# Kernel tuning notes

Hardware: AMD Instinct MI355X
Metric: run time of the kernel (lower is better)

The kernel has to match this reference:

```python
import jax, jax.numpy as jnp
import numpy as np
from jax import lax

PAD = 960          # tf.pad amount each side
LN_EPS = 1e-3      # keras LayerNormalization default epsilon


def _process(x, h, gamma, beta):
    """SmallConvNet: grouped 1D conv (per-channel learnable kernel) -> LayerNorm -> SiLU.
    x: (B, 2, 64), h: (2, 961) -> (B, 2, 1024). Dropout omitted (see notes)."""
    # grouped conv: each of the 2 'sequence' channels has its own length-961 kernel
    y = lax.conv_general_dilated(
        x, h[:, None, :],                 # kernel (O=2, I=1, W=961)
        window_strides=(1,), padding=[(PAD, PAD)],
        dimension_numbers=("NCH", "OIH", "NCH"),
        feature_group_count=2)            # (B, 2, 1024)
    mu = jnp.mean(y, axis=-1, keepdims=True)
    var = jnp.mean(jnp.square(y - mu), axis=-1, keepdims=True)
    ln = gamma * (y - mu) * lax.rsqrt(var + LN_EPS) + beta
    return jax.nn.silu(ln)


def reference(values, h, gamma, beta, symbols):
    # values: (B, 2, 64); symbols: (2, 64)
    vp = _process(values, h, gamma, beta)                              # (B, 2, 1024)
    sp = _process(jnp.zeros_like(values) + symbols, h, gamma, beta)    # (B, 2, 1024)
    # sign-based cosine-similarity attention: S[b,i,j] = mean_d sign(vp[b,j,d])*sign(vp[b,j,d]+sp[b,i,d])
    Xi = vp[:, None, :, :]   # (B, 1, N, D)
    Xj = sp[:, :, None, :]   # (B, N, 1, D)
    S = jnp.mean(jnp.sign(Xi) * jnp.sign(Xi + Xj), axis=-1)           # (B, N, N)
    scores = jax.nn.softmax(S, axis=-1)
    attn = jnp.einsum("bij,bjd->bid", scores, vp)                     # (B, N, D)
    return jax.nn.silu(attn * sp)


def setup_inputs() -> dict:
    key = jax.random.key(0)
    k1, k2, k3 = jax.random.split(key, 3)
    B, N, Din, D = 16384, 2, 64, 1024
    return {
        "values": jax.random.normal(k1, (B, N, Din), dtype=jnp.float32),
        "h": jax.random.normal(k2, (2, 961), dtype=jnp.float32),
        "gamma": jnp.ones((D,), dtype=jnp.float32),
        "beta": jnp.zeros((D,), dtype=jnp.float32),
        "symbols": jax.random.normal(k3, (N, Din), dtype=jnp.float32),
    }
```

## Files before the change

kernel.cpp:

```cpp
#include <hip/hip_runtime.h>

#define LN_EPS 1e-3f

typedef __attribute__((ext_vector_type(8))) short bf16x8;
typedef __attribute__((ext_vector_type(4))) float f32x4;

static __device__ __forceinline__ float sgnf(float x) {
    return (x > 0.f) ? 1.f : ((x < 0.f) ? -1.f : 0.f);
}
static __device__ __forceinline__ float siluf(float x) {
    return x * __builtin_amdgcn_rcpf(1.f + __expf(-x));
}

static __device__ __forceinline__ unsigned short f2bf(float f) {
    unsigned int u = __float_as_uint(f);
    return (unsigned short)((u + 0x7fffu + ((u >> 16) & 1u)) >> 16);
}
static __device__ __forceinline__ float bf2f(unsigned short s) {
    return __uint_as_float(((unsigned int)s) << 16);
}
static __device__ __forceinline__ void split3(float v, unsigned short& hi,
                                              unsigned short& mid, unsigned short& lo) {
    hi = f2bf(v);
    const float r1 = v - bf2f(hi);
    mid = f2bf(r1);
    const float r2 = r1 - bf2f(mid);
    lo = f2bf(r2);
}

#define SPOFF 196608

__global__ __launch_bounds__(256) void hd_prep_sp(
    const float* __restrict__ h, const float* __restrict__ symbols,
    const float* __restrict__ gamma, const float* __restrict__ beta,
    float* __restrict__ ws)
{
    __shared__ float h_pad[2][1088];
    __shared__ float x_s[2][64];
    __shared__ float red[4][2];
    const int t = threadIdx.x;

    for (int idx = t; idx < 2 * 1088; idx += 256) {
        const int c = idx / 1088, j = idx - c * 1088;
        float v = 0.f;
        if (j >= 63 && j <= 1023) v = h[c * 961 + (j - 63)];
        h_pad[c][j] = v;
    }
    if (t < 128) x_s[t >> 6][t & 63] = symbols[t];
    __syncthreads();

    const int c = t >> 7, tt = t & 127;
    const int lane = t & 63, wid = t >> 6;
    const int jbase = 1023 - tt;

    float acc[8];
    #pragma unroll
    for (int k = 0; k < 8; ++k) acc[k] = 0.f;

    #pragma unroll 8
    for (int i = 0; i < 64; ++i) {
        const float xv = x_s[c][i];
        #pragma unroll
        for (int k = 0; k < 8; ++k)
            acc[k] = fmaf(xv, h_pad[c][jbase + i - 128 * k], acc[k]);
    }

    float ps = 0.f, pq = 0.f;
    #pragma unroll
    for (int k = 0; k < 8; ++k) { ps += acc[k]; pq += acc[k] * acc[k]; }
    #pragma unroll
    for (int off = 32; off; off >>= 1) {
        ps += __shfl_xor(ps, off);
        pq += __shfl_xor(pq, off);
    }
    if (lane == 0) { red[wid][0] = ps; red[wid][1] = pq; }
    __syncthreads();

    const float sum = red[2 * c][0] + red[2 * c + 1][0];
    const float sq  = red[2 * c][1] + red[2 * c + 1][1];
    const float mu  = sum * (1.f / 1024.f);
    float var = sq * (1.f / 1024.f) - mu * mu;
    var = fmaxf(var, 0.f);
    const float rs = rsqrtf(var + LN_EPS);

    #pragma unroll
    for (int k = 0; k < 8; ++k) {
        const int d = tt + 128 * k;
        const float ln = (acc[k] - mu) * rs * gamma[d] + beta[d];
        ws[SPOFF + c * 1024 + d] = siluf(ln);
    }
}

__global__ __launch_bounds__(256) void hd_prep_bpack(
    const float* __restrict__ h, float* __restrict__ ws)
{
    unsigned short* Bp = (unsigned short*)ws;
    const int total = 2 * 2 * 64 * 64 * 8;
    for (int e = blockIdx.x * 256 + threadIdx.x; e < total; e += gridDim.x * 256) {
        const int j   = e & 7;
        const int l   = (e >> 3) & 63;
        const int ntg = (e >> 9) & 63;
        const int ks  = (e >> 15) & 1;
        const int c   = (e >> 16) & 1;
        const int H = 1023 - (16 * ntg + (l & 15)) + 32 * ks + 8 * (l >> 4) + j;
        float v = 0.f;
        if (H >= 63 && H <= 1023) v = h[c * 961 + (H - 63)];
        unsigned short hi, mid, lo;
        split3(v, hi, mid, lo);
        const int T = (c * 2 + ks) * 64 + ntg;
        Bp[((T * 192 +   0 + l)) * 8 + j] = hi;
        Bp[((T * 192 +  64 + l)) * 8 + j] = mid;
        Bp[((T * 192 + 128 + l)) * 8 + j] = lo;
    }
}

__global__ __launch_bounds__(1024, 4) void hd_main_mfma(
    const float* __restrict__ values,
    const float* __restrict__ gamma, const float* __restrict__ beta,
    const float* __restrict__ ws, float* __restrict__ out)
{
    __shared__ __align__(16) unsigned short a_lds[2][2][3][16][40];
    __shared__ float stats[16][4][2][4][2];
    __shared__ float statsF[64];
    __shared__ int   sredF [64];
    __shared__ float otile[16][4][72];

    const int t = threadIdx.x;
    const int w = t >> 6, l = t & 63;
    const int g = l >> 4, q = l & 15;
    const int b0 = blockIdx.x * 16;

    if (t < 64) sredF[t] = 0;

    {
        const float2 xv2 = *reinterpret_cast<const float2*>(
            values + (size_t)b0 * 128 + 2 * t);
        #pragma unroll
        for (int u = 0; u < 2; ++u) {
            const int v  = 2 * t + u;
            const int q_ = v >> 7, c_ = (v >> 6) & 1, k_ = v & 63;
            const int ks_ = k_ >> 5, gj = k_ & 31;
            unsigned short hb, mb, lb;
            split3(u == 0 ? xv2.x : xv2.y, hb, mb, lb);
            a_lds[c_][ks_][0][q_][gj] = hb;
            a_lds[c_][ks_][1][q_][gj] = mb;
            a_lds[c_][ks_][2][q_][gj] = lb;
        }
    }
    __syncthreads();

    bf16x8 ahi[2][2], amd_[2][2], alo[2][2];
    #pragma unroll
    for (int c = 0; c < 2; ++c)
        #pragma unroll
        for (int ks = 0; ks < 2; ++ks) {
            ahi[c][ks]  = *reinterpret_cast<const bf16x8*>(&a_lds[c][ks][0][q][8 * g]);
            amd_[c][ks] = *reinterpret_cast<const bf16x8*>(&a_lds[c][ks][1][q][8 * g]);
            alo[c][ks]  = *reinterpret_cast<const bf16x8*>(&a_lds[c][ks][2][q][8 * g]);
        }

    const bf16x8* Bv = reinterpret_cast<const bf16x8*>(ws) + l;
    f32x4 acc[2][4];
    #pragma unroll
    for (int c = 0; c < 2; ++c)
        #pragma unroll
        for (int nt = 0; nt < 4; ++nt)
            acc[c][nt] = (f32x4){0.f, 0.f, 0.f, 0.f};

    __builtin_amdgcn_s_setprio(1);
    #pragma unroll
    for (int nt = 0; nt < 4; ++nt) {
        const int ntg = w * 4 + nt;
        #pragma unroll
        for (int c = 0; c < 2; ++c) {
            f32x4 ts = {0.f, 0.f, 0.f, 0.f};
            f32x4 tm = {0.f, 0.f, 0.f, 0.f};
            f32x4 th = {0.f, 0.f, 0.f, 0.f};
            #pragma unroll
            for (int ks = 0; ks < 2; ++ks) {
                const bf16x8* p = Bv + (size_t)((c * 2 + ks) * 64 + ntg) * 192;
                const bf16x8 bh = p[0], bm = p[64], bl = p[128];
                ts = __builtin_amdgcn_mfma_f32_16x16x32_bf16(amd_[c][ks], bl, ts, 0, 0, 0);
                ts = __builtin_amdgcn_mfma_f32_16x16x32_bf16(alo[c][ks], bm, ts, 0, 0, 0);
                ts = __builtin_amdgcn_mfma_f32_16x16x32_bf16(ahi[c][ks], bl, ts, 0, 0, 0);
                ts = __builtin_amdgcn_mfma_f32_16x16x32_bf16(amd_[c][ks], bm, ts, 0, 0, 0);
                ts = __builtin_amdgcn_mfma_f32_16x16x32_bf16(alo[c][ks], bh, ts, 0, 0, 0);
                tm = __builtin_amdgcn_mfma_f32_16x16x32_bf16(ahi[c][ks], bm, tm, 0, 0, 0);
                tm = __builtin_amdgcn_mfma_f32_16x16x32_bf16(amd_[c][ks], bh, tm, 0, 0, 0);
                th = __builtin_amdgcn_mfma_f32_16x16x32_bf16(ahi[c][ks], bh, th, 0, 0, 0);
            }
            #pragma unroll
            for (int r = 0; r < 4; ++r)
                acc[c][nt][r] = (ts[r] + tm[r]) + th[r];
        }
    }
    __builtin_amdgcn_s_setprio(0);

    {
        float s_[2][4], q_[2][4];
        #pragma unroll
        for (int c = 0; c < 2; ++c)
            #pragma unroll
            for (int r = 0; r < 4; ++r) { s_[c][r] = 0.f; q_[c][r] = 0.f; }
        #pragma unroll
        for (int c = 0; c < 2; ++c)
            #pragma unroll
            for (int nt = 0; nt < 4; ++nt)
                #pragma unroll
                for (int r = 0; r < 4; ++r) {
                    const float v = acc[c][nt][r];
                    s_[c][r] += v;
                    q_[c][r] += v * v;
                }
        #pragma unroll
        for (int off = 1; off < 16; off <<= 1)
            #pragma unroll
            for (int c = 0; c < 2; ++c)
                #pragma unroll
                for (int r = 0; r < 4; ++r) {
                    s_[c][r] += __shfl_xor(s_[c][r], off);
                    q_[c][r] += __shfl_xor(q_[c][r], off);
                }
        if (q == 0) {
            #pragma unroll
            for (int c = 0; c < 2; ++c)
                #pragma unroll
                for (int r = 0; r < 4; ++r) {
                    stats[w][g][c][r][0] = s_[c][r];
                    stats[w][g][c][r][1] = q_[c][r];
                }
        }
    }
    __syncthreads();
    if (t < 64) {
        const int gg = t >> 4, cc = (t >> 3) & 1, rr = (t >> 1) & 3, ss = t & 1;
        float S = 0.f;
        #pragma unroll
        for (int w2 = 0; w2 < 16; ++w2) S += stats[w2][gg][cc][rr][ss];
        statsF[t] = S;
    }
    __syncthreads();

    float mu_[2][4], rs_[2][4];
    #pragma unroll
    for (int c = 0; c < 2; ++c)
        #pragma unroll
        for (int r = 0; r < 4; ++r) {
            const float S = statsF[((g * 2 + c) * 4 + r) * 2 + 0];
            const float Q = statsF[((g * 2 + c) * 4 + r) * 2 + 1];
            const float mu = S * (1.f / 1024.f);
            float var = Q * (1.f / 1024.f) - mu * mu;
            var = fmaxf(var, 0.f);
            mu_[c][r] = mu;
            rs_[c][r] = rsqrtf(var + LN_EPS);
        }

    const int dbase = w * 64 + q;
    #pragma unroll
    for (int nt = 0; nt < 4; ++nt) {
        const int d = dbase + 16 * nt;
        const float gam = gamma[d];
        const float bet = beta[d];
        #pragma unroll
        for (int c = 0; c < 2; ++c)
            #pragma unroll
            for (int r = 0; r < 4; ++r)
                acc[c][nt][r] = siluf((acc[c][nt][r] - mu_[c][r]) * rs_[c][r] * gam + bet);
    }

    float spv[2][4];
    #pragma unroll
    for (int nt = 0; nt < 4; ++nt) {
        const int d = dbase + 16 * nt;
        spv[0][nt] = ws[SPOFF + d];
        spv[1][nt] = ws[SPOFF + 1024 + d];
    }

    int cnt[2][4][2];
    #pragma unroll
    for (int c = 0; c < 2; ++c)
        #pragma unroll
        for (int r = 0; r < 4; ++r) { cnt[c][r][0] = 0; cnt[c][r][1] = 0; }
    #pragma unroll
    for (int nt = 0; nt < 4; ++nt) {
        #pragma unroll
        for (int c = 0; c < 2; ++c)
            #pragma unroll
            for (int r = 0; r < 4; ++r) {
                const float v = acc[c][nt][r];
                const unsigned int iv = __float_as_uint(v);
                cnt[c][r][0] += (int)((iv ^ __float_as_uint(v + spv[0][nt])) >> 31);
                cnt[c][r][1] += (int)((iv ^ __float_as_uint(v + spv[1][nt])) >> 31);
            }
    }
    #pragma unroll
    for (int off = 1; off < 16; off <<= 1)
        #pragma unroll
        for (int c = 0; c < 2; ++c)
            #pragma unroll
            for (int r = 0; r < 4; ++r) {
                cnt[c][r][0] += __shfl_xor(cnt[c][r][0], off);
                cnt[c][r][1] += __shfl_xor(cnt[c][r][1], off);
            }
    if (q == 0) {
        #pragma unroll
        for (int c = 0; c < 2; ++c)
            #pragma unroll
            for (int r = 0; r < 4; ++r) {
                atomicAdd(&sredF[((g * 2 + c) * 4 + r) * 2 + 0], cnt[c][r][0]);
                atomicAdd(&sredF[((g * 2 + c) * 4 + r) * 2 + 1], cnt[c][r][1]);
            }
    }
    __syncthreads();

    float p0_[4][2], p1_[4][2];
    #pragma unroll
    for (int r = 0; r < 4; ++r)
        #pragma unroll
        for (int a = 0; a < 2; ++a) {
            const int t0 = sredF[((g * 2 + 0) * 4 + r) * 2 + a];
            const int t1 = sredF[((g * 2 + 1) * 4 + r) * 2 + a];
            const float S0 = 1.f - 2.f * (float)t0 * (1.f / 1024.f);
            const float S1 = 1.f - 2.f * (float)t1 * (1.f / 1024.f);
            const float m  = fmaxf(S0, S1);
            const float e0 = __expf(S0 - m), e1 = __expf(S1 - m);
            const float inv = __builtin_amdgcn_rcpf(e0 + e1);
            p0_[r][a] = e0 * inv;
            p1_[r][a] = e1 * inv;
        }

    const int g2 = l >> 4, qq = l & 15;
    #pragma unroll
    for (int a = 0; a < 2; ++a) {
        #pragma unroll
        for (int r = 0; r < 4; ++r) {
            #pragma unroll
            for (int nt = 0; nt < 4; ++nt) {
                const float attn = p0_[r][a] * acc[0][nt][r] + p1_[r][a] * acc[1][nt][r];
                otile[w][g][16 * nt + q] = siluf(attn * spv[a][nt]);
            }
            __builtin_amdgcn_wave_barrier();
            const float4 v4 = *reinterpret_cast<const float4*>(&otile[w][g2][4 * qq]);
            *reinterpret_cast<float4*>(
                out + ((size_t)(b0 + 4 * g2 + r) * 2 + a) * 1024 + 64 * w + 4 * qq) = v4;
            __builtin_amdgcn_wave_barrier();
        }
    }
}

__global__ __launch_bounds__(256) void hd_prep_scalar(
    const float* __restrict__ h, const float* __restrict__ symbols,
    const float* __restrict__ gamma, const float* __restrict__ beta,
    float* __restrict__ ws)
{
    __shared__ float h_pad[2][1088];
    __shared__ float x_s[2][64];
    __shared__ float red[4][2];
    const int t = threadIdx.x;

    for (int idx = t; idx < 2 * 1088; idx += 256) {
        const int c = idx / 1088, j = idx - c * 1088;
        float v = 0.f;
        if (j >= 63 && j <= 1023) v = h[c * 961 + (j - 63)];
        h_pad[c][j] = v;
        const int src = 1086 - j;
        float vr = 0.f;
        if (src >= 63 && src <= 1023) vr = h[c * 961 + (src - 63)];
        ws[c * 1088 + j] = vr;
    }
    if (t < 128) x_s[t >> 6][t & 63] = symbols[t];
    __syncthreads();

    const int c = t >> 7, tt = t & 127;
    const int lane = t & 63, wid = t >> 6;
    const int jbase = 1023 - tt;

    float acc[8];
    #pragma unroll
    for (int k = 0; k < 8; ++k) acc[k] = 0.f;

    #pragma unroll 8
    for (int i = 0; i < 64; ++i) {
        const float xv = x_s[c][i];
        #pragma unroll
        for (int k = 0; k < 8; ++k)
            acc[k] = fmaf(xv, h_pad[c][jbase + i - 128 * k], acc[k]);
    }

    float ps = 0.f, pq = 0.f;
    #pragma unroll
    for (int k = 0; k < 8; ++k) { ps += acc[k]; pq += acc[k] * acc[k]; }
    #pragma unroll
    for (int off = 32; off; off >>= 1) {
        ps += __shfl_xor(ps, off);
        pq += __shfl_xor(pq, off);
    }
    if (lane == 0) { red[wid][0] = ps; red[wid][1] = pq; }
    __syncthreads();

    const float sum = red[2 * c][0] + red[2 * c + 1][0];
    const float sq  = red[2 * c][1] + red[2 * c + 1][1];
    const float mu  = sum * (1.f / 1024.f);
    float var = sq * (1.f / 1024.f) - mu * mu;
    var = fmaxf(var, 0.f);
    const float rs = rsqrtf(var + LN_EPS);

    #pragma unroll
    for (int k = 0; k < 8; ++k) {
        const int d = tt + 128 * k;
        const float ln = (acc[k] - mu) * rs * gamma[d] + beta[d];
        ws[2176 + c * 1024 + d] = siluf(ln);
    }
}

__global__ __launch_bounds__(256, 4) void hd_main_scalar(
    const float* __restrict__ values,
    const float* __restrict__ gamma, const float* __restrict__ beta,
    const float* __restrict__ ws, float* __restrict__ out)
{
    __shared__ float hrev[2][1088];
    __shared__ float red[4][16];
    __shared__ float redf[16];
    __shared__ float red2[4][16];
    __shared__ float redf2[16];

    const int t = threadIdx.x;
    const int lane = t & 63, wid = t >> 6;
    const size_t b0 = (size_t)blockIdx.x * 4;

    for (int idx = t; idx < 2 * 1088; idx += 256)
        (&hrev[0][0])[idx] = ws[idx];
    __syncthreads();

    float acc[4][2][4];
    #pragma unroll
    for (int b = 0; b < 4; ++b)
        #pragma unroll
        for (int c = 0; c < 2; ++c)
            #pragma unroll
            for (int k = 0; k < 4; ++k) acc[b][c][k] = 0.f;

    #pragma unroll 1
    for (int i0 = 0; i0 < 64; i0 += 8) {
        const int q0 = 56 + 4 * t - i0;
        float r[2][12];
        #pragma unroll
        for (int c = 0; c < 2; ++c) {
            const float4* p = reinterpret_cast<const float4*>(&hrev[c][q0]);
            const float4 a0 = p[0], a1 = p[1], a2 = p[2];
            r[c][0] = a0.x; r[c][1] = a0.y; r[c][2]  = a0.z; r[c][3]  = a0.w;
            r[c][4] = a1.x; r[c][5] = a1.y; r[c][6]  = a1.z; r[c][7]  = a1.w;
            r[c][8] = a2.x; r[c][9] = a2.y; r[c][10] = a2.z; r[c][11] = a2.w;
        }
        #pragma unroll
        for (int b = 0; b < 4; ++b) {
            #pragma unroll
            for (int c = 0; c < 2; ++c) {
                const float* xp = values + ((b0 + b) * 2 + c) * 64 + i0;
                #pragma unroll
                for (int il = 0; il < 8; ++il) {
                    const float xv = xp[il];
                    #pragma unroll
                    for (int k = 0; k < 4; ++k)
                        acc[b][c][k] = fmaf(xv, r[c][7 - il + k], acc[b][c][k]);
                }
            }
        }
    }

    {
        float v16[16];
        #pragma unroll
        for (int b = 0; b < 4; ++b)
            #pragma unroll
            for (int c = 0; c < 2; ++c) {
                const float a0 = acc[b][c][0], a1 = acc[b][c][1];
                const float a2 = acc[b][c][2], a3 = acc[b][c][3];
                v16[(b * 2 + c) * 2]     = a0 + a1 + a2 + a3;
                v16[(b * 2 + c) * 2 + 1] = a0 * a0 + a1 * a1 + a2 * a2 + a3 * a3;
            }
        #pragma unroll
        for (int off = 32; off; off >>= 1)
            #pragma unroll
            for (int v = 0; v < 16; ++v)
                v16[v] += __shfl_xor(v16[v], off);
        if (lane == 0) {
            #pragma unroll
            for (int v = 0; v < 16; ++v) red[wid][v] = v16[v];
        }
    }
    __syncthreads();
    if (t < 16) redf[t] = red[0][t] + red[1][t] + red[2][t] + red[3][t];
    __syncthreads();

    const float4 g4  = *reinterpret_cast<const float4*>(&gamma[4 * t]);
    const float4 be4 = *reinterpret_cast<const float4*>(&beta[4 * t]);
    float sp_r[2][4];
    #pragma unroll
    for (int a = 0; a < 2; ++a) {
        const float4 s4 = *reinterpret_cast<const float4*>(&ws[2176 + a * 1024 + 4 * t]);
        sp_r[a][0] = s4.x; sp_r[a][1] = s4.y; sp_r[a][2] = s4.z; sp_r[a][3] = s4.w;
    }
    const float gk[4] = {g4.x, g4.y, g4.z, g4.w};
    const float bk[4] = {be4.x, be4.y, be4.z, be4.w};

    #pragma unroll
    for (int b = 0; b < 4; ++b)
        #pragma unroll
        for (int c = 0; c < 2; ++c) {
            const float sum = redf[(b * 2 + c) * 2];
            const float sq  = redf[(b * 2 + c) * 2 + 1];
            const float mu  = sum * (1.f / 1024.f);
            float var = sq * (1.f / 1024.f) - mu * mu;
            var = fmaxf(var, 0.f);
            const float rs = rsqrtf(var + LN_EPS);
            #pragma unroll
            for (int k = 0; k < 4; ++k)
                acc[b][c][k] = siluf((acc[b][c][k] - mu) * rs * gk[k] + bk[k]);
        }

    {
        float v16[16];
        #pragma unroll
        for (int b = 0; b < 4; ++b)
            #pragma unroll
            for (int a = 0; a < 2; ++a)
                #pragma unroll
                for (int c = 0; c < 2; ++c) {
                    float s = 0.f;
                    #pragma unroll
                    for (int k = 0; k < 4; ++k)
                        s += sgnf(acc[b][c][k]) * sgnf(acc[b][c][k] + sp_r[a][k]);
                    v16[b * 4 + a * 2 + c] = s;
                }
        #pragma unroll
        for (int off = 32; off; off >>= 1)
            #pragma unroll
            for (int v = 0; v < 16; ++v)
                v16[v] += __shfl_xor(v16[v], off);
        if (lane == 0) {
            #pragma unroll
            for (int v = 0; v < 16; ++v) red2[wid][v] = v16[v];
        }
    }
    __syncthreads();
    if (t < 16) redf2[t] = red2[0][t] + red2[1][t] + red2[2][t] + red2[3][t];
    __syncthreads();

    #pragma unroll
    for (int b = 0; b < 4; ++b) {
        #pragma unroll
        for (int a = 0; a < 2; ++a) {
            const float s0 = redf2[b * 4 + a * 2 + 0] * (1.f / 1024.f);
            const float s1 = redf2[b * 4 + a * 2 + 1] * (1.f / 1024.f);
            const float m  = fmaxf(s0, s1);
            const float e0 = __expf(s0 - m), e1 = __expf(s1 - m);
            const float inv = 1.f / (e0 + e1);
            const float p0 = e0 * inv, p1 = e1 * inv;
            float4 o;
            o.x = siluf((p0 * acc[b][0][0] + p1 * acc[b][1][0]) * sp_r[a][0]);
            o.y = siluf((p0 * acc[b][0][1] + p1 * acc[b][1][1]) * sp_r[a][1]);
            o.z = siluf((p0 * acc[b][0][2] + p1 * acc[b][1][2]) * sp_r[a][2]);
            o.w = siluf((p0 * acc[b][0][3] + p1 * acc[b][1][3]) * sp_r[a][3]);
            *reinterpret_cast<float4*>(out + ((b0 + b) * 2 + a) * 1024 + 4 * t) = o;
        }
    }
}

extern "C" void kernel_launch(void* const* d_in, const int* in_sizes, int n_in,
                              void* d_out, int out_size, void* d_ws, size_t ws_size,
                              hipStream_t stream) {
    const float* values  = (const float*)d_in[0];
    const float* h       = (const float*)d_in[1];
    const float* gamma   = (const float*)d_in[2];
    const float* beta    = (const float*)d_in[3];
    const float* symbols = (const float*)d_in[4];
    float* out = (float*)d_out;
    float* ws  = (float*)d_ws;

    const int B = in_sizes[0] / 128;

    if (ws_size >= 794624) {
        hipLaunchKernelGGL(hd_prep_sp, dim3(1), dim3(256), 0, stream,
                           h, symbols, gamma, beta, ws);
        hipLaunchKernelGGL(hd_prep_bpack, dim3(256), dim3(256), 0, stream, h, ws);
        hipLaunchKernelGGL(hd_main_mfma, dim3(B / 16), dim3(1024), 0, stream,
                           values, gamma, beta, ws, out);
    } else {
        hipLaunchKernelGGL(hd_prep_scalar, dim3(1), dim3(256), 0, stream,
                           h, symbols, gamma, beta, ws);
        hipLaunchKernelGGL(hd_main_scalar, dim3(B / 4), dim3(256), 0, stream,
                           values, gamma, beta, ws, out);
    }
}
```

Before: 107.6 us.

## Process two 16-row batch sub-tiles per block to reuse packed B fragments

Each block now handles 32 batch rows as two 16-row sub-tiles, so every B-fragment load from the packed kernel workspace feeds twice as many MFMAs, and the grid is halved. A fragments are now read from LDS inside the loop rather than held in registers, and the LayerNorm statistics and sign-count reductions are doubled. A dummy 6200-float LDS pad array, touched through an opaque asm read, inflates shared memory use, apparently to cap blocks per CU. The change trades extra accumulator registers and LDS traffic for fewer global loads, fewer launches and larger per-block work.

```diff
diff --git a/kernel.cpp b/kernel.cpp
--- a/kernel.cpp
+++ b/kernel.cpp
@@ -119,53 +119,54 @@
     const float* __restrict__ gamma, const float* __restrict__ beta,
     const float* __restrict__ ws, float* __restrict__ out)
 {
-    __shared__ __align__(16) unsigned short a_lds[2][2][3][16][40];
-    __shared__ float stats[16][4][2][4][2];
-    __shared__ float statsF[64];
-    __shared__ int   sredF [64];
+    __shared__ __align__(16) unsigned short a_lds[2][2][2][3][16][40];
+    __shared__ float stats[16][4][2][2][4][2];
+    __shared__ float statsF[128];
+    __shared__ int   sredF [128];
     __shared__ float otile[16][4][72];
+    __shared__ float lds_pad[6200];
 
     const int t = threadIdx.x;
     const int w = t >> 6, l = t & 63;
     const int g = l >> 4, q = l & 15;
-    const int b0 = blockIdx.x * 16;
-
-    if (t < 64) sredF[t] = 0;
-
+    const int b0 = blockIdx.x * 32;
+
+    lds_pad[t] = (float)(int)blockIdx.x;
     {
-        const float2 xv2 = *reinterpret_cast<const float2*>(
-            values + (size_t)b0 * 128 + 2 * t);
-        #pragma unroll
-        for (int u = 0; u < 2; ++u) {
-            const int v  = 2 * t + u;
-            const int q_ = v >> 7, c_ = (v >> 6) & 1, k_ = v & 63;
+        float pv = lds_pad[(t * 37) & 4095];
+        asm volatile("" : : "v"(pv));
+    }
+
+    if (t < 128) sredF[t] = 0;
+
+    {
+        const float4 xv4 = *reinterpret_cast<const float4*>(
+            values + (size_t)b0 * 128 + 4 * t);
+        const float xs[4] = {xv4.x, xv4.y, xv4.z, xv4.w};
+        #pragma unroll
+        for (int u = 0; u < 4; ++u) {
+            const int v  = 4 * t + u;
+            const int bs = v >> 11;
+            const int q_ = (v >> 7) & 15, c_ = (v >> 6) & 1, k_ = v & 63;
             const int ks_ = k_ >> 5, gj = k_ & 31;
             unsigned short hb, mb, lb;
-            split3(u == 0 ? xv2.x : xv2.y, hb, mb, lb);
-            a_lds[c_][ks_][0][q_][gj] = hb;
-            a_lds[c_][ks_][1][q_][gj] = mb;
-            a_lds[c_][ks_][2][q_][gj] = lb;
-        }
-    }
-    __syncthreads();
-
-    bf16x8 ahi[2][2], amd_[2][2], alo[2][2];
-    #pragma unroll
-    for (int c = 0; c < 2; ++c)
-        #pragma unroll
-        for (int ks = 0; ks < 2; ++ks) {
-            ahi[c][ks]  = *reinterpret_cast<const bf16x8*>(&a_lds[c][ks][0][q][8 * g]);
-            amd_[c][ks] = *reinterpret_cast<const bf16x8*>(&a_lds[c][ks][1][q][8 * g]);
-            alo[c][ks]  = *reinterpret_cast<const bf16x8*>(&a_lds[c][ks][2][q][8 * g]);
-        }
+            split3(xs[u], hb, mb, lb);
+            a_lds[bs][c_][ks_][0][q_][gj] = hb;
+            a_lds[bs][c_][ks_][1][q_][gj] = mb;
+            a_lds[bs][c_][ks_][2][q_][gj] = lb;
+        }
+    }
+    __syncthreads();
 
     const bf16x8* Bv = reinterpret_cast<const bf16x8*>(ws) + l;
-    f32x4 acc[2][4];
-    #pragma unroll
-    for (int c = 0; c < 2; ++c)
-        #pragma unroll
-        for (int nt = 0; nt < 4; ++nt)
-            acc[c][nt] = (f32x4){0.f, 0.f, 0.f, 0.f};
+    f32x4 acc[2][2][4];
+    #pragma unroll
+    for (int bs = 0; bs < 2; ++bs)
+        #pragma unroll
+        for (int c = 0; c < 2; ++c)
+            #pragma unroll
+            for (int nt = 0; nt < 4; ++nt)
+                acc[bs][c][nt] = (f32x4){0.f, 0.f, 0.f, 0.f};
 
     __builtin_amdgcn_s_setprio(1);
     #pragma unroll
@@ -173,30 +174,49 @@
         const int ntg = w * 4 + nt;
         #pragma unroll
         for (int c = 0; c < 2; ++c) {
-            f32x4 ts = {0.f, 0.f, 0.f, 0.f};
-            f32x4 tm = {0.f, 0.f, 0.f, 0.f};
-            f32x4 th = {0.f, 0.f, 0.f, 0.f};
-            #pragma unroll
-            for (int ks = 0; ks < 2; ++ks) {
-                const bf16x8* p = Bv + (size_t)((c * 2 + ks) * 64 + ntg) * 192;
-                const bf16x8 bh = p[0], bm = p[64], bl = p[128];
-                ts = __builtin_amdgcn_mfma_f32_16x16x32_bf16(amd_[c][ks], bl, ts, 0, 0, 0);
-                ts = __builtin_amdgcn_mfma_f32_16x16x32_bf16(alo[c][ks], bm, ts, 0, 0, 0);
-                ts = __builtin_amdgcn_mfma_f32_16x16x32_bf16(ahi[c][ks], bl, ts, 0, 0, 0);
-                ts = __builtin_amdgcn_mfma_f32_16x16x32_bf16(amd_[c][ks], bm, ts, 0, 0, 0);
-                ts = __builtin_amdgcn_mfma_f32_16x16x32_bf16(alo[c][ks], bh, ts, 0, 0, 0);
-                tm = __builtin_amdgcn_mfma_f32_16x16x32_bf16(ahi[c][ks], bm, tm, 0, 0, 0);
-                tm = __builtin_amdgcn_mfma_f32_16x16x32_bf16(amd_[c][ks], bh, tm, 0, 0, 0);
-                th = __builtin_amdgcn_mfma_f32_16x16x32_bf16(ahi[c][ks], bh, th, 0, 0, 0);
+            const bf16x8* p0 = Bv + (size_t)((c * 2 + 0) * 64 + ntg) * 192;
+            const bf16x8* p1 = Bv + (size_t)((c * 2 + 1) * 64 + ntg) * 192;
+            const bf16x8 b0h = p0[0], b0m = p0[64], b0l = p0[128];
+            const bf16x8 b1h = p1[0], b1m = p1[64], b1l = p1[128];
+            #pragma unroll
+            for (int bs = 0; bs < 2; ++bs) {
+                f32x4 ts = {0.f, 0.f, 0.f, 0.f};
+                f32x4 tm = {0.f, 0.f, 0.f, 0.f};
+                f32x4 th = {0.f, 0.f, 0.f, 0.f};
+                {
+                    const bf16x8 a_h = *reinterpret_cast<const bf16x8*>(&a_lds[bs][c][0][0][q][8 * g]);
+                    const bf16x8 a_m = *reinterpret_cast<const bf16x8*>(&a_lds[bs][c][0][1][q][8 * g]);
+                    const bf16x8 a_l = *reinterpret_cast<const bf16x8*>(&a_lds[bs][c][0][2][q][8 * g]);
+                    ts = __builtin_amdgcn_mfma_f32_16x16x32_bf16(a_m, b0l, ts, 0, 0, 0);
+                    ts = __builtin_amdgcn_mfma_f32_16x16x32_bf16(a_l, b0m, ts, 0, 0, 0);
+                    ts = __builtin_amdgcn_mfma_f32_16x16x32_bf16(a_h, b0l, ts, 0, 0, 0);
+                    ts = __builtin_amdgcn_mfma_f32_16x16x32_bf16(a_m, b0m, ts, 0, 0, 0);
+                    ts = __builtin_amdgcn_mfma_f32_16x16x32_bf16(a_l, b0h, ts, 0, 0, 0);
+                    tm = __builtin_amdgcn_mfma_f32_16x16x32_bf16(a_h, b0m, tm, 0, 0, 0);
+                    tm = __builtin_amdgcn_mfma_f32_16x16x32_bf16(a_m, b0h, tm, 0, 0, 0);
+                    th = __builtin_amdgcn_mfma_f32_16x16x32_bf16(a_h, b0h, th, 0, 0, 0);
+                }
+                {
+                    const bf16x8 a_h = *reinterpret_cast<const bf16x8*>(&a_lds[bs][c][1][0][q][8 * g]);
+                    const bf16x8 a_m = *reinterpret_cast<const bf16x8*>(&a_lds[bs][c][1][1][q][8 * g]);
+                    const bf16x8 a_l = *reinterpret_cast<const bf16x8*>(&a_lds[bs][c][1][2][q][8 * g]);
+                    ts = __builtin_amdgcn_mfma_f32_16x16x32_bf16(a_m, b1l, ts, 0, 0, 0);
+                    ts = __builtin_amdgcn_mfma_f32_16x16x32_bf16(a_l, b1m, ts, 0, 0, 0);
+                    ts = __builtin_amdgcn_mfma_f32_16x16x32_bf16(a_h, b1l, ts, 0, 0, 0);
+                    ts = __builtin_amdgcn_mfma_f32_16x16x32_bf16(a_m, b1m, ts, 0, 0, 0);
+                    ts = __builtin_amdgcn_mfma_f32_16x16x32_bf16(a_l, b1h, ts, 0, 0, 0);
+                    tm = __builtin_amdgcn_mfma_f32_16x16x32_bf16(a_h, b1m, tm, 0, 0, 0);
+                    tm = __builtin_amdgcn_mfma_f32_16x16x32_bf16(a_m, b1h, tm, 0, 0, 0);
+                    th = __builtin_amdgcn_mfma_f32_16x16x32_bf16(a_h, b1h, th, 0, 0, 0);
+                }
+                acc[bs][c][nt] = (ts + tm) + th;
             }
-            #pragma unroll
-            for (int r = 0; r < 4; ++r)
-                acc[c][nt][r] = (ts[r] + tm[r]) + th[r];
         }
     }
     __builtin_amdgcn_s_setprio(0);
 
-    {
+    #pragma unroll
+    for (int bs = 0; bs < 2; ++bs) {
         float s_[2][4], q_[2][4];
         #pragma unroll
         for (int c = 0; c < 2; ++c)
@@ -208,7 +228,7 @@
             for (int nt = 0; nt < 4; ++nt)
                 #pragma unroll
                 for (int r = 0; r < 4; ++r) {
-                    const float v = acc[c][nt][r];
+                    const float v = acc[bs][c][nt][r];
                     s_[c][r] += v;
                     q_[c][r] += v * v;
                 }
@@ -226,34 +246,38 @@
             for (int c = 0; c < 2; ++c)
                 #pragma unroll
                 for (int r = 0; r < 4; ++r) {
-                    stats[w][g][c][r][0] = s_[c][r];
-                    stats[w][g][c][r][1] = q_[c][r];
-                }
-        }
-    }
-    __syncthreads();
-    if (t < 64) {
-        const int gg = t >> 4, cc = (t >> 3) & 1, rr = (t >> 1) & 3, ss = t & 1;
+                    stats[w][g][bs][c][r][0] = s_[c][r];
+                    stats[w][g][bs][c][r][1] = q_[c][r];
+                }
+        }
+    }
+    __syncthreads();
+    if (t < 128) {
+        const int gg = t >> 5, bs_ = (t >> 4) & 1, cc = (t >> 3) & 1;
+        const int rr = (t >> 1) & 3, ss = t & 1;
         float S = 0.f;
         #pragma unroll
-        for (int w2 = 0; w2 < 16; ++w2) S += stats[w2][gg][cc][rr][ss];
+        for (int w2 = 0; w2 < 16; ++w2) S += stats[w2][gg][bs_][cc][rr][ss];
         statsF[t] = S;
     }
     __syncthreads();
 
-    float mu_[2][4], rs_[2][4];
-    #pragma unroll
-    for (int c = 0; c < 2; ++c)
-        #pragma unroll
-        for (int r = 0; r < 4; ++r) {
-            const float S = statsF[((g * 2 + c) * 4 + r) * 2 + 0];
-            const float Q = statsF[((g * 2 + c) * 4 + r) * 2 + 1];
-            const float mu = S * (1.f / 1024.f);
-            float var = Q * (1.f / 1024.f) - mu * mu;
-            var = fmaxf(var, 0.f);
-            mu_[c][r] = mu;
-            rs_[c][r] = rsqrtf(var + LN_EPS);
-        }
+    float mu_[2][2][4], rs_[2][2][4];
+    #pragma unroll
+    for (int bs = 0; bs < 2; ++bs)
+        #pragma unroll
+        for (int c = 0; c < 2; ++c)
+            #pragma unroll
+            for (int r = 0; r < 4; ++r) {
+                const int base = g * 32 + bs * 16 + c * 8 + r * 2;
+                const float S = statsF[base];
+                const float Q = statsF[base + 1];
+                const float mu = S * (1.f / 1024.f);
+                float var = Q * (1.f / 1024.f) - mu * mu;
+                var = fmaxf(var, 0.f);
+                mu_[bs][c][r] = mu;
+                rs_[bs][c][r] = rsqrtf(var + LN_EPS);
+            }
 
     const int dbase = w * 64 + q;
     #pragma unroll
@@ -262,10 +286,13 @@
         const float gam = gamma[d];
         const float bet = beta[d];
         #pragma unroll
-        for (int c = 0; c < 2; ++c)
-            #pragma unroll
-            for (int r = 0; r < 4; ++r)
-                acc[c][nt][r] = siluf((acc[c][nt][r] - mu_[c][r]) * rs_[c][r] * gam + bet);
+        for (int bs = 0; bs < 2; ++bs)
+            #pragma unroll
+            for (int c = 0; c < 2; ++c)
+                #pragma unroll
+                for (int r = 0; r < 4; ++r)
+                    acc[bs][c][nt][r] =
+                        siluf((acc[bs][c][nt][r] - mu_[bs][c][r]) * rs_[bs][c][r] * gam + bet);
     }
 
     float spv[2][4];
@@ -276,74 +303,85 @@
         spv[1][nt] = ws[SPOFF + 1024 + d];
     }
 
-    int cnt[2][4][2];
-    #pragma unroll
-    for (int c = 0; c < 2; ++c)
-        #pragma unroll
-        for (int r = 0; r < 4; ++r) { cnt[c][r][0] = 0; cnt[c][r][1] = 0; }
-    #pragma unroll
-    for (int nt = 0; nt < 4; ++nt) {
+    #pragma unroll
+    for (int bs = 0; bs < 2; ++bs) {
+        int cnt[2][4][2];
         #pragma unroll
         for (int c = 0; c < 2; ++c)
             #pragma unroll
+            for (int r = 0; r < 4; ++r) { cnt[c][r][0] = 0; cnt[c][r][1] = 0; }
+        #pragma unroll
+        for (int nt = 0; nt < 4; ++nt) {
+            #pragma unroll
+            for (int c = 0; c < 2; ++c)
+                #pragma unroll
+                for (int r = 0; r < 4; ++r) {
+                    const float v = acc[bs][c][nt][r];
+                    const unsigned int iv = __float_as_uint(v);
+                    cnt[c][r][0] += (int)((iv ^ __float_as_uint(v + spv[0][nt])) >> 31);
+                    cnt[c][r][1] += (int)((iv ^ __float_as_uint(v + spv[1][nt])) >> 31);
+                }
+        }
+        #pragma unroll
+        for (int off = 1; off < 16; off <<= 1)
+            #pragma unroll
+            for (int c = 0; c < 2; ++c)
+                #pragma unroll
+                for (int r = 0; r < 4; ++r) {
+                    cnt[c][r][0] += __shfl_xor(cnt[c][r][0], off);
+                    cnt[c][r][1] += __shfl_xor(cnt[c][r][1], off);
+                }
+        if (q == 0) {
+            #pragma unroll
+            for (int c = 0; c < 2; ++c)
+                #pragma unroll
+                for (int r = 0; r < 4; ++r) {
+                    const int base = g * 32 + bs * 16 + c * 8 + r * 2;
+                    atomicAdd(&sredF[base + 0], cnt[c][r][0]);
+                    atomicAdd(&sredF[base + 1], cnt[c][r][1]);
+                }
+        }
+    }
+    __syncthreads();
+
+    float p0_[2][4][2], p1_[2][4][2];
+    #pragma unroll
+    for (int bs = 0; bs < 2; ++bs)
+        #pragma unroll
+        for (int r = 0; r < 4; ++r)
+            #pragma unroll
+            for (int a = 0; a < 2; ++a) {
+                const int t0 = sredF[g * 32 + bs * 16 + 0 + r * 2 + a];
+                const int t1 = sredF[g * 32 + bs * 16 + 8 + r * 2 + a];
+                const float S0 = 1.f - 2.f * (float)t0 * (1.f / 1024.f);
+                const float S1 = 1.f - 2.f * (float)t1 * (1.f / 1024.f);
+                const float m  = fmaxf(S0, S1);
+                const float e0 = __expf(S0 - m), e1 = __expf(S1 - m);
+                const float inv = __builtin_amdgcn_rcpf(e0 + e1);
+                p0_[bs][r][a] = e0 * inv;
+                p1_[bs][r][a] = e1 * inv;
+            }
+
+    const int g2 = l >> 4, qq = l & 15;
+    #pragma unroll
+    for (int bs = 0; bs < 2; ++bs) {
+        #pragma unroll
+        for (int a = 0; a < 2; ++a) {
+            #pragma unroll
             for (int r = 0; r < 4; ++r) {
-                const float v = acc[c][nt][r];
-                const unsigned int iv = __float_as_uint(v);
-                cnt[c][r][0] += (int)((iv ^ __float_as_uint(v + spv[0][nt])) >> 31);
-                cnt[c][r][1] += (int)((iv ^ __float_as_uint(v + spv[1][nt])) >> 31);
+                #pragma unroll
+                for (int nt = 0; nt < 4; ++nt) {
+                    const float attn = p0_[bs][r][a] * acc[bs][0][nt][r]
+                                     + p1_[bs][r][a] * acc[bs][1][nt][r];
+                    otile[w][g][16 * nt + q] = siluf(attn * spv[a][nt]);
+                }
+                __builtin_amdgcn_wave_barrier();
+                const float4 v4 = *reinterpret_cast<const float4*>(&otile[w][g2][4 * qq]);
+                *reinterpret_cast<float4*>(
+                    out + ((size_t)(b0 + 16 * bs + 4 * g2 + r) * 2 + a) * 1024
+                        + 64 * w + 4 * qq) = v4;
+                __builtin_amdgcn_wave_barrier();
             }
-    }
-    #pragma unroll
-    for (int off = 1; off < 16; off <<= 1)
-        #pragma unroll
-        for (int c = 0; c < 2; ++c)
-            #pragma unroll
-            for (int r = 0; r < 4; ++r) {
-                cnt[c][r][0] += __shfl_xor(cnt[c][r][0], off);
-                cnt[c][r][1] += __shfl_xor(cnt[c][r][1], off);
-            }
-    if (q == 0) {
-        #pragma unroll
-        for (int c = 0; c < 2; ++c)
-            #pragma unroll
-            for (int r = 0; r < 4; ++r) {
-                atomicAdd(&sredF[((g * 2 + c) * 4 + r) * 2 + 0], cnt[c][r][0]);
-                atomicAdd(&sredF[((g * 2 + c) * 4 + r) * 2 + 1], cnt[c][r][1]);
-            }
-    }
-    __syncthreads();
-
-    float p0_[4][2], p1_[4][2];
-    #pragma unroll
-    for (int r = 0; r < 4; ++r)
-        #pragma unroll
-        for (int a = 0; a < 2; ++a) {
-            const int t0 = sredF[((g * 2 + 0) * 4 + r) * 2 + a];
-            const int t1 = sredF[((g * 2 + 1) * 4 + r) * 2 + a];
-            const float S0 = 1.f - 2.f * (float)t0 * (1.f / 1024.f);
-            const float S1 = 1.f - 2.f * (float)t1 * (1.f / 1024.f);
-            const float m  = fmaxf(S0, S1);
-            const float e0 = __expf(S0 - m), e1 = __expf(S1 - m);
-            const float inv = __builtin_amdgcn_rcpf(e0 + e1);
-            p0_[r][a] = e0 * inv;
-            p1_[r][a] = e1 * inv;
-        }
-
-    const int g2 = l >> 4, qq = l & 15;
-    #pragma unroll
-    for (int a = 0; a < 2; ++a) {
-        #pragma unroll
-        for (int r = 0; r < 4; ++r) {
-            #pragma unroll
-            for (int nt = 0; nt < 4; ++nt) {
-                const float attn = p0_[r][a] * acc[0][nt][r] + p1_[r][a] * acc[1][nt][r];
-                otile[w][g][16 * nt + q] = siluf(attn * spv[a][nt]);
-            }
-            __builtin_amdgcn_wave_barrier();
-            const float4 v4 = *reinterpret_cast<const float4*>(&otile[w][g2][4 * qq]);
-            *reinterpret_cast<float4*>(
-                out + ((size_t)(b0 + 4 * g2 + r) * 2 + a) * 1024 + 64 * w + 4 * qq) = v4;
-            __builtin_amdgcn_wave_barrier();
         }
     }
 }
@@ -584,7 +622,7 @@
         hipLaunchKernelGGL(hd_prep_sp, dim3(1), dim3(256), 0, stream,
                            h, symbols, gamma, beta, ws);
         hipLaunchKernelGGL(hd_prep_bpack, dim3(256), dim3(256), 0, stream, h, ws);
-        hipLaunchKernelGGL(hd_main_mfma, dim3(B / 16), dim3(1024), 0, stream,
+        hipLaunchKernelGGL(hd_main_mfma, dim3(B / 32), dim3(1024), 0, stream,
                            values, gamma, beta, ws, out);
     } else {
         hipLaunchKernelGGL(hd_prep_scalar, dim3(1), dim3(256), 0, stream,
```

Result: slower. 176.8 us (+64.3%).
